# Kernel optimization log

Hardware: AMD Instinct MI355X
Metric: run time of the kernel (lower is better)

## Reference

```python
import jax, jax.numpy as jnp
import numpy as np

B, N, IN_DIM, OUT_DIM = 8, 2048, 128, 64
TEMPERATURE = 1.0
NEG_SLOPE = 0.2


def setup_inputs() -> dict:
    key = jax.random.key(0)
    k1, k2, k3, k4, k5 = jax.random.split(key, 5)
    s_fc = 1.0 / np.sqrt(IN_DIM)
    s_at = 1.0 / np.sqrt(2 * OUT_DIM)
    return {
        "h": jax.random.normal(k1, (B, N, IN_DIM), dtype=jnp.float32),
        "W_fc": jax.random.normal(k2, (IN_DIM, OUT_DIM), dtype=jnp.float32) * s_fc,
        "b_fc": jax.random.normal(k3, (OUT_DIM,), dtype=jnp.float32) * s_fc,
        "a_src": jax.random.normal(k4, (OUT_DIM,), dtype=jnp.float32) * s_at,
        "a_dst": jax.random.normal(k5, (OUT_DIM,), dtype=jnp.float32) * s_at,
        "b_attn": jnp.zeros((), dtype=jnp.float32),
    }


def reference(h, W_fc, b_fc, a_src, a_dst, b_attn):
    # hp: (B, N, OUT_DIM) -- projected node features
    hp = h @ W_fc + b_fc
    # attn_fc(concat(h_i, h_j)) == h_i@a_src + h_j@a_dst + b (exact decomposition)
    s = hp @ a_src  # (B, N) source contribution
    d = hp @ a_dst  # (B, N) dest contribution
    scores = s[:, :, None] + d[:, None, :] + b_attn  # (B, N, N)
    scores = jnp.where(scores >= 0, scores, NEG_SLOPE * scores)  # leaky_relu
    scores = scores / TEMPERATURE
    attn = jax.nn.softmax(scores, axis=-1)
    out = jnp.einsum("bij,bjd->bid", attn, hp)
    return jax.nn.elu(out)
```

## Files before the change

kernel.cpp:

```cpp
#include <hip/hip_runtime.h>
#include <hip/hip_bf16.h>
#include <math.h>

#define BB 8
#define NN 2048
#define IND 128
#define OUTD 64
#define NEG 0.2f

typedef __attribute__((ext_vector_type(8))) short short8;
typedef __attribute__((ext_vector_type(4))) float f32x4;

__device__ __forceinline__ unsigned short f2bf(float f) {
    unsigned int u = __float_as_uint(f);
    u += 0x7fffu + ((u >> 16) & 1u);
    return (unsigned short)(u >> 16);
}

__device__ __forceinline__ unsigned int pk_bf16(float a, float b) {
    union { __hip_bfloat162 h; unsigned int u; } cv;
    cv.h = __float22bfloat162_rn(make_float2(a, b));
    return cv.u;
}

__global__ __launch_bounds__(256) void gat_proj_kernel(
    const float* __restrict__ h, const float* __restrict__ W,
    const float* __restrict__ bfc, const float* __restrict__ asrc,
    const float* __restrict__ adst,
    unsigned short* __restrict__ hpT2, float* __restrict__ s,
    float* __restrict__ F, float* __restrict__ H)
{
    __shared__ float Wl[IND * OUTD];
    __shared__ float hl[64 * 132];

    const int t  = threadIdx.x;
    const int R0 = blockIdx.x * 64;

    const float4* W4 = (const float4*)W;
    float4*       Wl4 = (float4*)Wl;
    #pragma unroll
    for (int k2 = 0; k2 < 8; ++k2) Wl4[t + k2 * 256] = W4[t + k2 * 256];

    const float4* h4 = (const float4*)(h + (size_t)R0 * IND);
    #pragma unroll
    for (int k2 = 0; k2 < 8; ++k2) {
        const int idx = t + k2 * 256;
        const int row = idx >> 5, c4 = idx & 31;
        *(float4*)&hl[row * 132 + c4 * 4] = h4[idx];
    }
    __syncthreads();

    const int r0 = (t >> 4) * 4;
    const int o0 = (t & 15) * 4;
    const float4 bias = *(const float4*)(bfc + o0);
    float4 a0 = bias, a1 = bias, a2 = bias, a3 = bias;

    #pragma unroll 2
    for (int kc = 0; kc < IND; kc += 4) {
        const float4 w0 = *(const float4*)&Wl[(kc + 0) * OUTD + o0];
        const float4 w1 = *(const float4*)&Wl[(kc + 1) * OUTD + o0];
        const float4 w2 = *(const float4*)&Wl[(kc + 2) * OUTD + o0];
        const float4 w3 = *(const float4*)&Wl[(kc + 3) * OUTD + o0];
        const float4 h0 = *(const float4*)&hl[(r0 + 0) * 132 + kc];
        const float4 h1 = *(const float4*)&hl[(r0 + 1) * 132 + kc];
        const float4 h2 = *(const float4*)&hl[(r0 + 2) * 132 + kc];
        const float4 h3 = *(const float4*)&hl[(r0 + 3) * 132 + kc];

        a0.x = fmaf(h0.x, w0.x, a0.x); a0.y = fmaf(h0.x, w0.y, a0.y);
        a0.z = fmaf(h0.x, w0.z, a0.z); a0.w = fmaf(h0.x, w0.w, a0.w);
        a0.x = fmaf(h0.y, w1.x, a0.x); a0.y = fmaf(h0.y, w1.y, a0.y);
        a0.z = fmaf(h0.y, w1.z, a0.z); a0.w = fmaf(h0.y, w1.w, a0.w);
        a0.x = fmaf(h0.z, w2.x, a0.x); a0.y = fmaf(h0.z, w2.y, a0.y);
        a0.z = fmaf(h0.z, w2.z, a0.z); a0.w = fmaf(h0.z, w2.w, a0.w);
        a0.x = fmaf(h0.w, w3.x, a0.x); a0.y = fmaf(h0.w, w3.y, a0.y);
        a0.z = fmaf(h0.w, w3.z, a0.z); a0.w = fmaf(h0.w, w3.w, a0.w);

        a1.x = fmaf(h1.x, w0.x, a1.x); a1.y = fmaf(h1.x, w0.y, a1.y);
        a1.z = fmaf(h1.x, w0.z, a1.z); a1.w = fmaf(h1.x, w0.w, a1.w);
        a1.x = fmaf(h1.y, w1.x, a1.x); a1.y = fmaf(h1.y, w1.y, a1.y);
        a1.z = fmaf(h1.y, w1.z, a1.z); a1.w = fmaf(h1.y, w1.w, a1.w);
        a1.x = fmaf(h1.z, w2.x, a1.x); a1.y = fmaf(h1.z, w2.y, a1.y);
        a1.z = fmaf(h1.z, w2.z, a1.z); a1.w = fmaf(h1.z, w2.w, a1.w);
        a1.x = fmaf(h1.w, w3.x, a1.x); a1.y = fmaf(h1.w, w3.y, a1.y);
        a1.z = fmaf(h1.w, w3.z, a1.z); a1.w = fmaf(h1.w, w3.w, a1.w);

        a2.x = fmaf(h2.x, w0.x, a2.x); a2.y = fmaf(h2.x, w0.y, a2.y);
        a2.z = fmaf(h2.x, w0.z, a2.z); a2.w = fmaf(h2.x, w0.w, a2.w);
        a2.x = fmaf(h2.y, w1.x, a2.x); a2.y = fmaf(h2.y, w1.y, a2.y);
        a2.z = fmaf(h2.y, w1.z, a2.z); a2.w = fmaf(h2.y, w1.w, a2.w);
        a2.x = fmaf(h2.z, w2.x, a2.x); a2.y = fmaf(h2.z, w2.y, a2.y);
        a2.z = fmaf(h2.z, w2.z, a2.z); a2.w = fmaf(h2.z, w2.w, a2.w);
        a2.x = fmaf(h2.w, w3.x, a2.x); a2.y = fmaf(h2.w, w3.y, a2.y);
        a2.z = fmaf(h2.w, w3.z, a2.z); a2.w = fmaf(h2.w, w3.w, a2.w);

        a3.x = fmaf(h3.x, w0.x, a3.x); a3.y = fmaf(h3.x, w0.y, a3.y);
        a3.z = fmaf(h3.x, w0.z, a3.z); a3.w = fmaf(h3.x, w0.w, a3.w);
        a3.x = fmaf(h3.y, w1.x, a3.x); a3.y = fmaf(h3.y, w1.y, a3.y);
        a3.z = fmaf(h3.y, w1.z, a3.z); a3.w = fmaf(h3.y, w1.w, a3.w);
        a3.x = fmaf(h3.z, w2.x, a3.x); a3.y = fmaf(h3.z, w2.y, a3.y);
        a3.z = fmaf(h3.z, w2.z, a3.z); a3.w = fmaf(h3.z, w2.w, a3.w);
        a3.x = fmaf(h3.w, w3.x, a3.x); a3.y = fmaf(h3.w, w3.y, a3.y);
        a3.z = fmaf(h3.w, w3.z, a3.z); a3.w = fmaf(h3.w, w3.w, a3.w);
    }

    const int b   = R0 >> 11;
    const int jb0 = (R0 & 2047) + r0;
    const int cj  = jb0 >> 3;
    const int sub = jb0 & 7;
    unsigned short* cbase = hpT2 + (((size_t)(b * 256 + cj)) * OUTD) * 8;
    {
        ushort4 v;
        v.x = f2bf(a0.x); v.y = f2bf(a1.x); v.z = f2bf(a2.x); v.w = f2bf(a3.x);
        *(ushort4*)(cbase + (o0 + 0) * 8 + sub) = v;
        v.x = f2bf(a0.y); v.y = f2bf(a1.y); v.z = f2bf(a2.y); v.w = f2bf(a3.y);
        *(ushort4*)(cbase + (o0 + 1) * 8 + sub) = v;
        v.x = f2bf(a0.z); v.y = f2bf(a1.z); v.z = f2bf(a2.z); v.w = f2bf(a3.z);
        *(ushort4*)(cbase + (o0 + 2) * 8 + sub) = v;
        v.x = f2bf(a0.w); v.y = f2bf(a1.w); v.z = f2bf(a2.w); v.w = f2bf(a3.w);
        *(ushort4*)(cbase + (o0 + 3) * 8 + sub) = v;
    }

    const float4 as4 = *(const float4*)(asrc + o0);
    const float4 ad4 = *(const float4*)(adst + o0);
    float vs[4], vd[4];
    vs[0] = a0.x*as4.x + a0.y*as4.y + a0.z*as4.z + a0.w*as4.w;
    vs[1] = a1.x*as4.x + a1.y*as4.y + a1.z*as4.z + a1.w*as4.w;
    vs[2] = a2.x*as4.x + a2.y*as4.y + a2.z*as4.z + a2.w*as4.w;
    vs[3] = a3.x*as4.x + a3.y*as4.y + a3.z*as4.z + a3.w*as4.w;
    vd[0] = a0.x*ad4.x + a0.y*ad4.y + a0.z*ad4.z + a0.w*ad4.w;
    vd[1] = a1.x*ad4.x + a1.y*ad4.y + a1.z*ad4.z + a1.w*ad4.w;
    vd[2] = a2.x*ad4.x + a2.y*ad4.y + a2.z*ad4.z + a2.w*ad4.w;
    vd[3] = a3.x*ad4.x + a3.y*ad4.y + a3.z*ad4.z + a3.w*ad4.w;
    #pragma unroll
    for (int msk = 1; msk <= 8; msk <<= 1) {
        #pragma unroll
        for (int r = 0; r < 4; ++r) {
            vs[r] += __shfl_xor(vs[r], msk);
            vd[r] += __shfl_xor(vd[r], msk);
        }
    }
    if ((t & 15) == 0) {
        #pragma unroll
        for (int r = 0; r < 4; ++r) {
            s[R0 + r0 + r] = vs[r];
            F[R0 + r0 + r] = __expf(vd[r]);
            H[R0 + r0 + r] = __expf(NEG * vd[r]);
        }
    }
}

__global__ __launch_bounds__(256) void gat_attn_kernel(
    const unsigned short* __restrict__ hpT2, const float* __restrict__ s,
    const float* __restrict__ F, const float* __restrict__ H,
    const float* __restrict__ battn_p, float* __restrict__ out)
{
    __shared__ float accl[4][16 * 65];
    __shared__ float ll[4][16];

    const int t    = threadIdx.x;
    const int lane = t & 63;
    const int wv   = t >> 6;
    const int tile = blockIdx.x;
    const int b    = tile >> 7;
    const int i0   = (tile & 127) * 16;
    const int m    = lane & 15;
    const int kc   = lane >> 4;

    const float battn = battn_p[0];
    const float sm = s[b * NN + i0 + m] + battn;
    const float Ei = __expf(sm);
    const float Gi = __expf(NEG * sm);
    const float* Fb = F + b * NN;
    const float* Hb = H + b * NN;
    const unsigned short* hb = hpT2 + (size_t)b * 256 * OUTD * 8;

    short8 ones;
    #pragma unroll
    for (int q = 0; q < 8; ++q) ones[q] = (short)0x3F80;

    f32x4 acc0 = {0.f, 0.f, 0.f, 0.f};
    f32x4 acc1 = {0.f, 0.f, 0.f, 0.f};
    f32x4 acc2 = {0.f, 0.f, 0.f, 0.f};
    f32x4 acc3 = {0.f, 0.f, 0.f, 0.f};
    f32x4 accl4 = {0.f, 0.f, 0.f, 0.f};

    const int jbase = wv * (NN / 4);

    #pragma unroll 2
    for (int it = 0; it < NN / 4 / 32; ++it) {
        const int j0 = jbase + it * 32;
        const float4 Fa = *(const float4*)(Fb + j0 + kc * 8);
        const float4 Fc = *(const float4*)(Fb + j0 + kc * 8 + 4);
        const float4 Ha = *(const float4*)(Hb + j0 + kc * 8);
        const float4 Hc = *(const float4*)(Hb + j0 + kc * 8 + 4);
        float wf[8];
        wf[0] = fmaxf(Ei * Fa.x, Gi * Ha.x);
        wf[1] = fmaxf(Ei * Fa.y, Gi * Ha.y);
        wf[2] = fmaxf(Ei * Fa.z, Gi * Ha.z);
        wf[3] = fmaxf(Ei * Fa.w, Gi * Ha.w);
        wf[4] = fmaxf(Ei * Fc.x, Gi * Hc.x);
        wf[5] = fmaxf(Ei * Fc.y, Gi * Hc.y);
        wf[6] = fmaxf(Ei * Fc.z, Gi * Hc.z);
        wf[7] = fmaxf(Ei * Fc.w, Gi * Hc.w);

        union { short8 s8; unsigned int u[4]; } af;
        af.u[0] = pk_bf16(wf[0], wf[1]);
        af.u[1] = pk_bf16(wf[2], wf[3]);
        af.u[2] = pk_bf16(wf[4], wf[5]);
        af.u[3] = pk_bf16(wf[6], wf[7]);

        const size_t cb = ((size_t)((j0 >> 3) + kc)) * OUTD * 8;
        const short8 bf0 = *(const short8*)(hb + cb + (0 * 16 + m) * 8);
        const short8 bf1 = *(const short8*)(hb + cb + (1 * 16 + m) * 8);
        const short8 bf2 = *(const short8*)(hb + cb + (2 * 16 + m) * 8);
        const short8 bf3 = *(const short8*)(hb + cb + (3 * 16 + m) * 8);

        acc0 = __builtin_amdgcn_mfma_f32_16x16x32_bf16(af.s8, bf0, acc0, 0, 0, 0);
        acc1 = __builtin_amdgcn_mfma_f32_16x16x32_bf16(af.s8, bf1, acc1, 0, 0, 0);
        acc2 = __builtin_amdgcn_mfma_f32_16x16x32_bf16(af.s8, bf2, acc2, 0, 0, 0);
        acc3 = __builtin_amdgcn_mfma_f32_16x16x32_bf16(af.s8, bf3, acc3, 0, 0, 0);
        accl4 = __builtin_amdgcn_mfma_f32_16x16x32_bf16(af.s8, ones, accl4, 0, 0, 0);
    }

    if (m == 0) {
        #pragma unroll
        for (int r = 0; r < 4; ++r) ll[wv][kc * 4 + r] = accl4[r];
    }

    #pragma unroll
    for (int r = 0; r < 4; ++r) {
        const int row = kc * 4 + r;
        accl[wv][row * 65 + 0 * 16 + m] = acc0[r];
        accl[wv][row * 65 + 1 * 16 + m] = acc1[r];
        accl[wv][row * 65 + 2 * 16 + m] = acc2[r];
        accl[wv][row * 65 + 3 * 16 + m] = acc3[r];
    }
    __syncthreads();

    const int col = t & 63;
    const int r0e = (t >> 6) * 4;
    float* ob = out + (((size_t)b * NN + i0) * OUTD);
    #pragma unroll
    for (int r = 0; r < 4; ++r) {
        const int row = r0e + r;
        const float lsum = (ll[0][row] + ll[1][row]) + (ll[2][row] + ll[3][row]);
        float v = (accl[0][row * 65 + col] + accl[1][row * 65 + col]) +
                  (accl[2][row * 65 + col] + accl[3][row * 65 + col]);
        v /= lsum;
        v = (v > 0.f) ? v : expm1f(v);
        ob[(size_t)row * OUTD + col] = v;
    }
}

extern "C" void kernel_launch(void* const* d_in, const int* in_sizes, int n_in,
                              void* d_out, int out_size, void* d_ws, size_t ws_size,
                              hipStream_t stream)
{
    const float* h     = (const float*)d_in[0];
    const float* W     = (const float*)d_in[1];
    const float* bfc   = (const float*)d_in[2];
    const float* asrc  = (const float*)d_in[3];
    const float* adst  = (const float*)d_in[4];
    const float* battn = (const float*)d_in[5];
    float* out = (float*)d_out;

    unsigned short* hpT2 = (unsigned short*)d_ws;
    float* s = (float*)((char*)d_ws + (size_t)BB * NN * OUTD * 2);
    float* F = s + (size_t)BB * NN;
    float* H = F + (size_t)BB * NN;

    gat_proj_kernel<<<(BB * NN) / 64, 256, 0, stream>>>(h, W, bfc, asrc, adst,
                                                        hpT2, s, F, H);
    gat_attn_kernel<<<BB * NN / 16, 256, 0, stream>>>(hpT2, s, F, H, battn, out);
}
```

Before: 93.45 us.

## Process four 16-row tiles per attention block to reuse hp fragments

The attention kernel now handles 64 query rows per block, four 16-row tiles per wave. Each loaded bf16 hp fragment and F/H vector feeds four sets of MFMA accumulators, cutting the cache traffic for re-reading the projected features by about four times. The cost is four times fewer blocks (256), more accumulator registers and a much larger LDS reduction buffer, which lowers occupancy and latency hiding. Separately, the projection kernel drops to 32 rows per block, doubling its block count to spread the small GEMM across more CUs.

```diff
diff --git a/kernel.cpp b/kernel.cpp
--- a/kernel.cpp
+++ b/kernel.cpp
@@ -31,10 +31,10 @@
     float* __restrict__ F, float* __restrict__ H)
 {
     __shared__ float Wl[IND * OUTD];
-    __shared__ float hl[64 * 132];
+    __shared__ float hl[32 * 132];
 
     const int t  = threadIdx.x;
-    const int R0 = blockIdx.x * 64;
+    const int R0 = blockIdx.x * 32;
 
     const float4* W4 = (const float4*)W;
     float4*       Wl4 = (float4*)Wl;
@@ -43,17 +43,17 @@
 
     const float4* h4 = (const float4*)(h + (size_t)R0 * IND);
     #pragma unroll
-    for (int k2 = 0; k2 < 8; ++k2) {
+    for (int k2 = 0; k2 < 4; ++k2) {
         const int idx = t + k2 * 256;
         const int row = idx >> 5, c4 = idx & 31;
         *(float4*)&hl[row * 132 + c4 * 4] = h4[idx];
     }
     __syncthreads();
 
-    const int r0 = (t >> 4) * 4;
+    const int r0 = (t >> 4) * 2;
     const int o0 = (t & 15) * 4;
     const float4 bias = *(const float4*)(bfc + o0);
-    float4 a0 = bias, a1 = bias, a2 = bias, a3 = bias;
+    float4 a0 = bias, a1 = bias;
 
     #pragma unroll 2
     for (int kc = 0; kc < IND; kc += 4) {
@@ -63,8 +63,6 @@
         const float4 w3 = *(const float4*)&Wl[(kc + 3) * OUTD + o0];
         const float4 h0 = *(const float4*)&hl[(r0 + 0) * 132 + kc];
         const float4 h1 = *(const float4*)&hl[(r0 + 1) * 132 + kc];
-        const float4 h2 = *(const float4*)&hl[(r0 + 2) * 132 + kc];
-        const float4 h3 = *(const float4*)&hl[(r0 + 3) * 132 + kc];
 
         a0.x = fmaf(h0.x, w0.x, a0.x); a0.y = fmaf(h0.x, w0.y, a0.y);
         a0.z = fmaf(h0.x, w0.z, a0.z); a0.w = fmaf(h0.x, w0.w, a0.w);
@@ -83,24 +81,6 @@
         a1.z = fmaf(h1.z, w2.z, a1.z); a1.w = fmaf(h1.z, w2.w, a1.w);
         a1.x = fmaf(h1.w, w3.x, a1.x); a1.y = fmaf(h1.w, w3.y, a1.y);
         a1.z = fmaf(h1.w, w3.z, a1.z); a1.w = fmaf(h1.w, w3.w, a1.w);
-
-        a2.x = fmaf(h2.x, w0.x, a2.x); a2.y = fmaf(h2.x, w0.y, a2.y);
-        a2.z = fmaf(h2.x, w0.z, a2.z); a2.w = fmaf(h2.x, w0.w, a2.w);
-        a2.x = fmaf(h2.y, w1.x, a2.x); a2.y = fmaf(h2.y, w1.y, a2.y);
-        a2.z = fmaf(h2.y, w1.z, a2.z); a2.w = fmaf(h2.y, w1.w, a2.w);
-        a2.x = fmaf(h2.z, w2.x, a2.x); a2.y = fmaf(h2.z, w2.y, a2.y);
-        a2.z = fmaf(h2.z, w2.z, a2.z); a2.w = fmaf(h2.z, w2.w, a2.w);
-        a2.x = fmaf(h2.w, w3.x, a2.x); a2.y = fmaf(h2.w, w3.y, a2.y);
-        a2.z = fmaf(h2.w, w3.z, a2.z); a2.w = fmaf(h2.w, w3.w, a2.w);
-
-        a3.x = fmaf(h3.x, w0.x, a3.x); a3.y = fmaf(h3.x, w0.y, a3.y);
-        a3.z = fmaf(h3.x, w0.z, a3.z); a3.w = fmaf(h3.x, w0.w, a3.w);
-        a3.x = fmaf(h3.y, w1.x, a3.x); a3.y = fmaf(h3.y, w1.y, a3.y);
-        a3.z = fmaf(h3.y, w1.z, a3.z); a3.w = fmaf(h3.y, w1.w, a3.w);
-        a3.x = fmaf(h3.z, w2.x, a3.x); a3.y = fmaf(h3.z, w2.y, a3.y);
-        a3.z = fmaf(h3.z, w2.z, a3.z); a3.w = fmaf(h3.z, w2.w, a3.w);
-        a3.x = fmaf(h3.w, w3.x, a3.x); a3.y = fmaf(h3.w, w3.y, a3.y);
-        a3.z = fmaf(h3.w, w3.z, a3.z); a3.w = fmaf(h3.w, w3.w, a3.w);
     }
 
     const int b   = R0 >> 11;
@@ -109,39 +89,34 @@
     const int sub = jb0 & 7;
     unsigned short* cbase = hpT2 + (((size_t)(b * 256 + cj)) * OUTD) * 8;
     {
-        ushort4 v;
-        v.x = f2bf(a0.x); v.y = f2bf(a1.x); v.z = f2bf(a2.x); v.w = f2bf(a3.x);
-        *(ushort4*)(cbase + (o0 + 0) * 8 + sub) = v;
-        v.x = f2bf(a0.y); v.y = f2bf(a1.y); v.z = f2bf(a2.y); v.w = f2bf(a3.y);
-        *(ushort4*)(cbase + (o0 + 1) * 8 + sub) = v;
-        v.x = f2bf(a0.z); v.y = f2bf(a1.z); v.z = f2bf(a2.z); v.w = f2bf(a3.z);
-        *(ushort4*)(cbase + (o0 + 2) * 8 + sub) = v;
-        v.x = f2bf(a0.w); v.y = f2bf(a1.w); v.z = f2bf(a2.w); v.w = f2bf(a3.w);
-        *(ushort4*)(cbase + (o0 + 3) * 8 + sub) = v;
+        ushort2 v;
+        v.x = f2bf(a0.x); v.y = f2bf(a1.x);
+        *(ushort2*)(cbase + (o0 + 0) * 8 + sub) = v;
+        v.x = f2bf(a0.y); v.y = f2bf(a1.y);
+        *(ushort2*)(cbase + (o0 + 1) * 8 + sub) = v;
+        v.x = f2bf(a0.z); v.y = f2bf(a1.z);
+        *(ushort2*)(cbase + (o0 + 2) * 8 + sub) = v;
+        v.x = f2bf(a0.w); v.y = f2bf(a1.w);
+        *(ushort2*)(cbase + (o0 + 3) * 8 + sub) = v;
     }
 
     const float4 as4 = *(const float4*)(asrc + o0);
     const float4 ad4 = *(const float4*)(adst + o0);
-    float vs[4], vd[4];
+    float vs[2], vd[2];
     vs[0] = a0.x*as4.x + a0.y*as4.y + a0.z*as4.z + a0.w*as4.w;
     vs[1] = a1.x*as4.x + a1.y*as4.y + a1.z*as4.z + a1.w*as4.w;
-    vs[2] = a2.x*as4.x + a2.y*as4.y + a2.z*as4.z + a2.w*as4.w;
-    vs[3] = a3.x*as4.x + a3.y*as4.y + a3.z*as4.z + a3.w*as4.w;
     vd[0] = a0.x*ad4.x + a0.y*ad4.y + a0.z*ad4.z + a0.w*ad4.w;
     vd[1] = a1.x*ad4.x + a1.y*ad4.y + a1.z*ad4.z + a1.w*ad4.w;
-    vd[2] = a2.x*ad4.x + a2.y*ad4.y + a2.z*ad4.z + a2.w*ad4.w;
-    vd[3] = a3.x*ad4.x + a3.y*ad4.y + a3.z*ad4.z + a3.w*ad4.w;
     #pragma unroll
     for (int msk = 1; msk <= 8; msk <<= 1) {
-        #pragma unroll
-        for (int r = 0; r < 4; ++r) {
-            vs[r] += __shfl_xor(vs[r], msk);
-            vd[r] += __shfl_xor(vd[r], msk);
-        }
+        vs[0] += __shfl_xor(vs[0], msk);
+        vs[1] += __shfl_xor(vs[1], msk);
+        vd[0] += __shfl_xor(vd[0], msk);
+        vd[1] += __shfl_xor(vd[1], msk);
     }
     if ((t & 15) == 0) {
         #pragma unroll
-        for (int r = 0; r < 4; ++r) {
+        for (int r = 0; r < 2; ++r) {
             s[R0 + r0 + r] = vs[r];
             F[R0 + r0 + r] = __expf(vd[r]);
             H[R0 + r0 + r] = __expf(NEG * vd[r]);
@@ -154,22 +129,26 @@
     const float* __restrict__ F, const float* __restrict__ H,
     const float* __restrict__ battn_p, float* __restrict__ out)
 {
-    __shared__ float accl[4][16 * 65];
-    __shared__ float ll[4][16];
+    __shared__ float accl[4][64 * 66];
+    __shared__ float ll[4][64];
 
     const int t    = threadIdx.x;
     const int lane = t & 63;
     const int wv   = t >> 6;
-    const int tile = blockIdx.x;
-    const int b    = tile >> 7;
-    const int i0   = (tile & 127) * 16;
+    const int blk  = blockIdx.x;
+    const int b    = blk >> 5;
+    const int i0   = (blk & 31) * 64;
     const int m    = lane & 15;
     const int kc   = lane >> 4;
 
     const float battn = battn_p[0];
-    const float sm = s[b * NN + i0 + m] + battn;
-    const float Ei = __expf(sm);
-    const float Gi = __expf(NEG * sm);
+    float E[4], G[4];
+    #pragma unroll
+    for (int T = 0; T < 4; ++T) {
+        const float smv = s[b * NN + i0 + T * 16 + m] + battn;
+        E[T] = __expf(smv);
+        G[T] = __expf(NEG * smv);
+    }
     const float* Fb = F + b * NN;
     const float* Hb = H + b * NN;
     const unsigned short* hb = hpT2 + (size_t)b * 256 * OUTD * 8;
@@ -178,74 +157,87 @@
     #pragma unroll
     for (int q = 0; q < 8; ++q) ones[q] = (short)0x3F80;
 
-    f32x4 acc0 = {0.f, 0.f, 0.f, 0.f};
-    f32x4 acc1 = {0.f, 0.f, 0.f, 0.f};
-    f32x4 acc2 = {0.f, 0.f, 0.f, 0.f};
-    f32x4 acc3 = {0.f, 0.f, 0.f, 0.f};
-    f32x4 accl4 = {0.f, 0.f, 0.f, 0.f};
+    f32x4 acc[4][4];
+    f32x4 dacc[4];
+    #pragma unroll
+    for (int T = 0; T < 4; ++T) {
+        dacc[T] = (f32x4){0.f, 0.f, 0.f, 0.f};
+        #pragma unroll
+        for (int ot = 0; ot < 4; ++ot) acc[T][ot] = (f32x4){0.f, 0.f, 0.f, 0.f};
+    }
 
     const int jbase = wv * (NN / 4);
 
     #pragma unroll 2
     for (int it = 0; it < NN / 4 / 32; ++it) {
         const int j0 = jbase + it * 32;
-        const float4 Fa = *(const float4*)(Fb + j0 + kc * 8);
-        const float4 Fc = *(const float4*)(Fb + j0 + kc * 8 + 4);
-        const float4 Ha = *(const float4*)(Hb + j0 + kc * 8);
-        const float4 Hc = *(const float4*)(Hb + j0 + kc * 8 + 4);
-        float wf[8];
-        wf[0] = fmaxf(Ei * Fa.x, Gi * Ha.x);
-        wf[1] = fmaxf(Ei * Fa.y, Gi * Ha.y);
-        wf[2] = fmaxf(Ei * Fa.z, Gi * Ha.z);
-        wf[3] = fmaxf(Ei * Fa.w, Gi * Ha.w);
-        wf[4] = fmaxf(Ei * Fc.x, Gi * Hc.x);
-        wf[5] = fmaxf(Ei * Fc.y, Gi * Hc.y);
-        wf[6] = fmaxf(Ei * Fc.z, Gi * Hc.z);
-        wf[7] = fmaxf(Ei * Fc.w, Gi * Hc.w);
-
-        union { short8 s8; unsigned int u[4]; } af;
-        af.u[0] = pk_bf16(wf[0], wf[1]);
-        af.u[1] = pk_bf16(wf[2], wf[3]);
-        af.u[2] = pk_bf16(wf[4], wf[5]);
-        af.u[3] = pk_bf16(wf[6], wf[7]);
-
         const size_t cb = ((size_t)((j0 >> 3) + kc)) * OUTD * 8;
         const short8 bf0 = *(const short8*)(hb + cb + (0 * 16 + m) * 8);
         const short8 bf1 = *(const short8*)(hb + cb + (1 * 16 + m) * 8);
         const short8 bf2 = *(const short8*)(hb + cb + (2 * 16 + m) * 8);
         const short8 bf3 = *(const short8*)(hb + cb + (3 * 16 + m) * 8);
 
-        acc0 = __builtin_amdgcn_mfma_f32_16x16x32_bf16(af.s8, bf0, acc0, 0, 0, 0);
-        acc1 = __builtin_amdgcn_mfma_f32_16x16x32_bf16(af.s8, bf1, acc1, 0, 0, 0);
-        acc2 = __builtin_amdgcn_mfma_f32_16x16x32_bf16(af.s8, bf2, acc2, 0, 0, 0);
-        acc3 = __builtin_amdgcn_mfma_f32_16x16x32_bf16(af.s8, bf3, acc3, 0, 0, 0);
-        accl4 = __builtin_amdgcn_mfma_f32_16x16x32_bf16(af.s8, ones, accl4, 0, 0, 0);
+        const float4 Fa = *(const float4*)(Fb + j0 + kc * 8);
+        const float4 Fc = *(const float4*)(Fb + j0 + kc * 8 + 4);
+        const float4 Ha = *(const float4*)(Hb + j0 + kc * 8);
+        const float4 Hc = *(const float4*)(Hb + j0 + kc * 8 + 4);
+
+        #pragma unroll
+        for (int T = 0; T < 4; ++T) {
+            const float Ei = E[T], Gi = G[T];
+            float wf[8];
+            wf[0] = fmaxf(Ei * Fa.x, Gi * Ha.x);
+            wf[1] = fmaxf(Ei * Fa.y, Gi * Ha.y);
+            wf[2] = fmaxf(Ei * Fa.z, Gi * Ha.z);
+            wf[3] = fmaxf(Ei * Fa.w, Gi * Ha.w);
+            wf[4] = fmaxf(Ei * Fc.x, Gi * Hc.x);
+            wf[5] = fmaxf(Ei * Fc.y, Gi * Hc.y);
+            wf[6] = fmaxf(Ei * Fc.z, Gi * Hc.z);
+            wf[7] = fmaxf(Ei * Fc.w, Gi * Hc.w);
+
+            union { short8 s8; unsigned int u[4]; } af;
+            af.u[0] = pk_bf16(wf[0], wf[1]);
+            af.u[1] = pk_bf16(wf[2], wf[3]);
+            af.u[2] = pk_bf16(wf[4], wf[5]);
+            af.u[3] = pk_bf16(wf[6], wf[7]);
+
+            acc[T][0] = __builtin_amdgcn_mfma_f32_16x16x32_bf16(af.s8, bf0, acc[T][0], 0, 0, 0);
+            acc[T][1] = __builtin_amdgcn_mfma_f32_16x16x32_bf16(af.s8, bf1, acc[T][1], 0, 0, 0);
+            acc[T][2] = __builtin_amdgcn_mfma_f32_16x16x32_bf16(af.s8, bf2, acc[T][2], 0, 0, 0);
+            acc[T][3] = __builtin_amdgcn_mfma_f32_16x16x32_bf16(af.s8, bf3, acc[T][3], 0, 0, 0);
+            dacc[T]   = __builtin_amdgcn_mfma_f32_16x16x32_bf16(af.s8, ones, dacc[T], 0, 0, 0);
+        }
     }
 
     if (m == 0) {
         #pragma unroll
-        for (int r = 0; r < 4; ++r) ll[wv][kc * 4 + r] = accl4[r];
-    }
-
-    #pragma unroll
-    for (int r = 0; r < 4; ++r) {
-        const int row = kc * 4 + r;
-        accl[wv][row * 65 + 0 * 16 + m] = acc0[r];
-        accl[wv][row * 65 + 1 * 16 + m] = acc1[r];
-        accl[wv][row * 65 + 2 * 16 + m] = acc2[r];
-        accl[wv][row * 65 + 3 * 16 + m] = acc3[r];
+        for (int T = 0; T < 4; ++T)
+            #pragma unroll
+            for (int r = 0; r < 4; ++r) ll[wv][T * 16 + kc * 4 + r] = dacc[T][r];
+    }
+
+    #pragma unroll
+    for (int T = 0; T < 4; ++T) {
+        #pragma unroll
+        for (int r = 0; r < 4; ++r) {
+            const int row = T * 16 + kc * 4 + r;
+            accl[wv][row * 66 + 0 * 16 + m] = acc[T][0][r];
+            accl[wv][row * 66 + 1 * 16 + m] = acc[T][1][r];
+            accl[wv][row * 66 + 2 * 16 + m] = acc[T][2][r];
+            accl[wv][row * 66 + 3 * 16 + m] = acc[T][3][r];
+        }
     }
     __syncthreads();
 
     const int col = t & 63;
-    const int r0e = (t >> 6) * 4;
+    const int r0e = (t >> 6) * 16;
     float* ob = out + (((size_t)b * NN + i0) * OUTD);
-    #pragma unroll
-    for (int r = 0; r < 4; ++r) {
+    #pragma unroll 4
+    for (int r = 0; r < 16; ++r) {
         const int row = r0e + r;
         const float lsum = (ll[0][row] + ll[1][row]) + (ll[2][row] + ll[3][row]);
-        float v = (accl[0][row * 65 + col] + accl[1][row * 65 + col]) +
-                  (accl[2][row * 65 + col] + accl[3][row * 65 + col]);
+        float v = (accl[0][row * 66 + col] + accl[1][row * 66 + col]) +
+                  (accl[2][row * 66 + col] + accl[3][row * 66 + col]);
         v /= lsum;
         v = (v > 0.f) ? v : expm1f(v);
         ob[(size_t)row * OUTD + col] = v;
@@ -269,7 +261,7 @@
     float* F = s + (size_t)BB * NN;
     float* H = F + (size_t)BB * NN;
 
-    gat_proj_kernel<<<(BB * NN) / 64, 256, 0, stream>>>(h, W, bfc, asrc, adst,
+    gat_proj_kernel<<<(BB * NN) / 32, 256, 0, stream>>>(h, W, bfc, asrc, adst,
                                                         hpT2, s, F, H);
-    gat_attn_kernel<<<BB * NN / 16, 256, 0, stream>>>(hpT2, s, F, H, battn, out);
-}
+    gat_attn_kernel<<<BB * (NN / 64), 256, 0, stream>>>(hpT2, s, F, H, battn, out);
+}
```

After: 91.56 us. 1.02x faster.
